# Optimization experiments

Measured on AMD Instinct MI355X. Metric: run time of the kernel, lower is better.

## Reference

```python
import jax, jax.numpy as jnp
import numpy as np


def setup_inputs() -> dict:
    key = jax.random.key(0)
    ks = jax.random.split(key, 7)
    B, C, H, W = 32, 512, 64, 64
    C8 = C // 8
    scale = 1.0 / np.sqrt(C)  # ~kaiming-ish for 1x1 conv
    return {
        "x": jax.random.normal(ks[0], (B, C, H, W), dtype=jnp.float32),
        "wq": jax.random.normal(ks[1], (C8, C), dtype=jnp.float32) * scale,
        "bq": jax.random.normal(ks[2], (C8,), dtype=jnp.float32) * 0.01,
        "wk": jax.random.normal(ks[3], (C8, C), dtype=jnp.float32) * scale,
        "bk": jax.random.normal(ks[4], (C8,), dtype=jnp.float32) * 0.01,
        "wv": jax.random.normal(ks[5], (C8, C), dtype=jnp.float32) * scale,
        "bv": jax.random.normal(ks[6], (C8,), dtype=jnp.float32) * 0.01,
    }


def reference(x, wq, bq, wk, bk, wv, bv):
    B, C, H, W = x.shape
    N = H * W
    xf = x.reshape(B, C, N)  # [B, C, N]
    # 1x1 convs == per-pixel linear projections C -> C//8
    q = jnp.einsum("bcn,oc->bon", xf, wq) + bq[None, :, None]  # [B, C8, N]
    k = jnp.einsum("bcn,oc->bon", xf, wk) + bk[None, :, None]  # [B, C8, N]
    v = jnp.einsum("bcn,oc->bon", xf, wv) + bv[None, :, None]  # [B, C8, N]
    # attention over channel pairs: [B, C8, C8], softmax over dim=-2 (rows)
    logits = jnp.einsum("bon,bpn->bop", q, k)
    attn = jax.nn.softmax(logits, axis=-2)
    out = jnp.einsum("bop,bpn->bon", attn, v)  # [B, C8, N]
    return out.mean(axis=-1)  # [B, C8]
```

## Files before the change

### kernel.cpp

```cpp
#include <hip/hip_runtime.h>


typedef __attribute__((ext_vector_type(8))) short short8;
typedef __attribute__((ext_vector_type(4))) float floatx4;
typedef __attribute__((ext_vector_type(4))) unsigned short ushort4v;

#define MFMA16(a, b, c) __builtin_amdgcn_mfma_f32_16x16x32_bf16((a), (b), (c), 0, 0, 0)

__device__ __forceinline__ unsigned short f2bf(float f) {
  unsigned int u = __float_as_uint(f);
  u = u + 0x7fffu + ((u >> 16) & 1u);
  return (unsigned short)(u >> 16);
}
__device__ __forceinline__ float bf2f(unsigned short h) {
  return __uint_as_float(((unsigned int)h) << 16);
}

constexpr int CB = 32;
constexpr int CC = 512;
constexpr int CO = 64;
constexpr int NN = 4096;
constexpr int NT = 128;
constexpr int KC = 32;
constexpr int NCH = CC / KC;

constexpr int XROW = 40;
constexpr int QROW = 72;

constexpr int WQH = 0;
constexpr int WQL = 2560;
constexpr int WKH = 5120;
constexpr int WKL = 7680;
constexpr int XHI = 10240;
constexpr int XLO = 15360;
constexpr int SMEM_U = 20480;
constexpr int QHI = 0, QLO = 4608, KHI = 9216, KLO = 13824;

__global__ __launch_bounds__(256, 2) void proj_kernel(
    const float* __restrict__ x, const float* __restrict__ wq,
    const float* __restrict__ bq, const float* __restrict__ wk,
    const float* __restrict__ bk, float* __restrict__ logits,
    float* __restrict__ xsum)
{
  __shared__ __align__(16) unsigned short smem[SMEM_U];

  const int t    = threadIdx.x;
  const int lane = t & 63;
  const int wave = t >> 6;
  const int quad = lane >> 4;
  const int l15  = lane & 15;
  const int b    = blockIdx.x >> 5;
  const int tile = blockIdx.x & 31;
  const int n0   = tile * NT;
  const int nlow = t & 31;
  const int chi  = t >> 5;

  floatx4 accq[4][2], acck[4][2];
#pragma unroll
  for (int mf = 0; mf < 4; ++mf)
#pragma unroll
    for (int nf = 0; nf < 2; ++nf) {
      accq[mf][nf] = (floatx4)0.0f;
      acck[mf][nf] = (floatx4)0.0f;
    }

  const float* xb = x + (size_t)b * CC * NN + n0;

  for (int ch = 0; ch < NCH; ++ch) {
    const int c0 = ch * KC;
    __syncthreads();

    float xs_part[4] = {0.f, 0.f, 0.f, 0.f};
#pragma unroll
    for (int i = 0; i < 4; ++i) {
      const int n = i * 32 + nlow;
      float v0 = xb[(size_t)(c0 + chi * 4 + 0) * NN + n];
      float v1 = xb[(size_t)(c0 + chi * 4 + 1) * NN + n];
      float v2 = xb[(size_t)(c0 + chi * 4 + 2) * NN + n];
      float v3 = xb[(size_t)(c0 + chi * 4 + 3) * NN + n];
      xs_part[0] += v0; xs_part[1] += v1; xs_part[2] += v2; xs_part[3] += v3;
      ushort4v h, l;
      h[0] = f2bf(v0); l[0] = f2bf(v0 - bf2f(h[0]));
      h[1] = f2bf(v1); l[1] = f2bf(v1 - bf2f(h[1]));
      h[2] = f2bf(v2); l[2] = f2bf(v2 - bf2f(h[2]));
      h[3] = f2bf(v3); l[3] = f2bf(v3 - bf2f(h[3]));
      *reinterpret_cast<ushort4v*>(&smem[XHI + n * XROW + chi * 4]) = h;
      *reinterpret_cast<ushort4v*>(&smem[XLO + n * XROW + chi * 4]) = l;
    }
#pragma unroll
    for (int j = 0; j < 4; ++j) {
      float v = xs_part[j];
      v += __shfl_xor(v, 16); v += __shfl_xor(v, 8);
      v += __shfl_xor(v, 4);  v += __shfl_xor(v, 2); v += __shfl_xor(v, 1);
      if ((lane & 31) == 0) atomicAdd(&xsum[b * CC + c0 + chi * 4 + j], v);
    }

#pragma unroll
    for (int i = 0; i < 2; ++i) {
      const int idx = t + i * 256;
      const int row = idx >> 3, cf = idx & 7;
      const floatx4 aq = *reinterpret_cast<const floatx4*>(
          &wq[(size_t)row * CC + c0 + cf * 4]);
      const floatx4 ak = *reinterpret_cast<const floatx4*>(
          &wk[(size_t)row * CC + c0 + cf * 4]);
      ushort4v qh, ql, kh, kl;
#pragma unroll
      for (int j = 0; j < 4; ++j) {
        qh[j] = f2bf(aq[j]); ql[j] = f2bf(aq[j] - bf2f(qh[j]));
        kh[j] = f2bf(ak[j]); kl[j] = f2bf(ak[j] - bf2f(kh[j]));
      }
      *reinterpret_cast<ushort4v*>(&smem[WQH + row * XROW + cf * 4]) = qh;
      *reinterpret_cast<ushort4v*>(&smem[WQL + row * XROW + cf * 4]) = ql;
      *reinterpret_cast<ushort4v*>(&smem[WKH + row * XROW + cf * 4]) = kh;
      *reinterpret_cast<ushort4v*>(&smem[WKL + row * XROW + cf * 4]) = kl;
    }
    __syncthreads();

    short8 xh[2], xl[2];
#pragma unroll
    for (int nf = 0; nf < 2; ++nf) {
      const int nr = wave * 32 + nf * 16 + l15;
      xh[nf] = *reinterpret_cast<const short8*>(&smem[XHI + nr * XROW + quad * 8]);
      xl[nf] = *reinterpret_cast<const short8*>(&smem[XLO + nr * XROW + quad * 8]);
    }
#pragma unroll
    for (int mf = 0; mf < 4; ++mf) {
      const int orow = mf * 16 + l15;
      const short8 aqh = *reinterpret_cast<const short8*>(&smem[WQH + orow * XROW + quad * 8]);
      const short8 aql = *reinterpret_cast<const short8*>(&smem[WQL + orow * XROW + quad * 8]);
      const short8 akh = *reinterpret_cast<const short8*>(&smem[WKH + orow * XROW + quad * 8]);
      const short8 akl = *reinterpret_cast<const short8*>(&smem[WKL + orow * XROW + quad * 8]);
#pragma unroll
      for (int nf = 0; nf < 2; ++nf) {
        accq[mf][nf] = MFMA16(aqh, xh[nf], accq[mf][nf]);
        accq[mf][nf] = MFMA16(aql, xh[nf], accq[mf][nf]);
        accq[mf][nf] = MFMA16(aqh, xl[nf], accq[mf][nf]);
        acck[mf][nf] = MFMA16(akh, xh[nf], acck[mf][nf]);
        acck[mf][nf] = MFMA16(akl, xh[nf], acck[mf][nf]);
        acck[mf][nf] = MFMA16(akh, xl[nf], acck[mf][nf]);
      }
    }
  }

#pragma unroll
  for (int mf = 0; mf < 4; ++mf)
#pragma unroll
    for (int r = 0; r < 4; ++r) {
      const int o = mf * 16 + quad * 4 + r;
      const float bqv = bq[o], bkv = bk[o];
#pragma unroll
      for (int nf = 0; nf < 2; ++nf) {
        accq[mf][nf][r] += bqv;
        acck[mf][nf][r] += bkv;
      }
    }

  floatx4 accS[4];
#pragma unroll
  for (int mf = 0; mf < 4; ++mf) accS[mf] = (floatx4)0.0f;

  for (int hh = 0; hh < 2; ++hh) {
    __syncthreads();
    if ((wave >> 1) == hh) {
      const int nbase = (wave & 1) * 32;
#pragma unroll
      for (int mf = 0; mf < 4; ++mf)
#pragma unroll
        for (int nf = 0; nf < 2; ++nf)
#pragma unroll
          for (int r = 0; r < 4; ++r) {
            const int o  = mf * 16 + quad * 4 + r;
            const int nc = nbase + nf * 16 + l15;
            const float qv = accq[mf][nf][r];
            const float kv = acck[mf][nf][r];
            const unsigned short qh = f2bf(qv);
            const unsigned short kh = f2bf(kv);
            smem[QHI + o * QROW + nc] = qh;
            smem[QLO + o * QROW + nc] = f2bf(qv - bf2f(qh));
            smem[KHI + o * QROW + nc] = kh;
            smem[KLO + o * QROW + nc] = f2bf(kv - bf2f(kh));
          }
    }
    __syncthreads();
#pragma unroll
    for (int ks = 0; ks < 2; ++ks) {
      const short8 bh = *reinterpret_cast<const short8*>(
          &smem[KHI + (wave * 16 + l15) * QROW + ks * 32 + quad * 8]);
      const short8 bl = *reinterpret_cast<const short8*>(
          &smem[KLO + (wave * 16 + l15) * QROW + ks * 32 + quad * 8]);
#pragma unroll
      for (int mf = 0; mf < 4; ++mf) {
        const short8 ah = *reinterpret_cast<const short8*>(
            &smem[QHI + (mf * 16 + l15) * QROW + ks * 32 + quad * 8]);
        const short8 al = *reinterpret_cast<const short8*>(
            &smem[QLO + (mf * 16 + l15) * QROW + ks * 32 + quad * 8]);
        accS[mf] = MFMA16(ah, bh, accS[mf]);
        accS[mf] = MFMA16(al, bh, accS[mf]);
        accS[mf] = MFMA16(ah, bl, accS[mf]);
      }
    }
  }

#pragma unroll
  for (int mf = 0; mf < 4; ++mf)
#pragma unroll
    for (int r = 0; r < 4; ++r) {
      const int o = mf * 16 + quad * 4 + r;
      const int p = wave * 16 + l15;
      atomicAdd(&logits[((size_t)b * CO + o) * CO + p], accS[mf][r]);
    }
}

__global__ __launch_bounds__(256) void zero_kernel(float* __restrict__ p, int n) {
  const int i = blockIdx.x * 256 + threadIdx.x;
  if (i < n) p[i] = 0.0f;
}

__global__ __launch_bounds__(256) void finalize_kernel(
    const float* __restrict__ wv, const float* __restrict__ bv,
    const float* __restrict__ logits, const float* __restrict__ xsum,
    float* __restrict__ out)
{
  __shared__ float ls[CO * 65];
  __shared__ float xs_s[CC];
  __shared__ float vbar_s[CO], w2_s[CO], cmax_s[CO];
  const int t = threadIdx.x;
  const int b = blockIdx.x;

  for (int i = t; i < CC; i += 256) xs_s[i] = xsum[b * CC + i];
#pragma unroll
  for (int i = 0; i < 16; ++i) {
    const int idx = t + i * 256;
    ls[(idx >> 6) * 65 + (idx & 63)] = logits[(size_t)b * CO * CO + idx];
  }
  __syncthreads();

  {
    const int p = t >> 2, part = t & 3;
    float s = 0.f;
    const float* wr = wv + (size_t)p * CC + part * 128;
    const float* xr = xs_s + part * 128;
#pragma unroll 4
    for (int c = 0; c < 128; ++c) s += wr[c] * xr[c];
    s += __shfl_xor(s, 1); s += __shfl_xor(s, 2);
    if (part == 0) vbar_s[p] = s * (1.0f / 4096.0f) + bv[p];
  }
  __syncthreads();

  if (t < CO) {
    float m = -1e30f;
    for (int o = 0; o < CO; ++o) m = fmaxf(m, ls[o * 65 + t]);
    float sum = 0.f;
    for (int o = 0; o < CO; ++o) sum += __expf(ls[o * 65 + t] - m);
    cmax_s[t] = m;
    w2_s[t]   = vbar_s[t] / sum;
  }
  __syncthreads();

  if (t < CO) {
    float acc = 0.f;
    for (int p = 0; p < CO; ++p)
      acc += __expf(ls[t * 65 + p] - cmax_s[p]) * w2_s[p];
    out[b * CO + t] = acc;
  }
}

extern "C" void kernel_launch(void* const* d_in, const int* in_sizes, int n_in,
                              void* d_out, int out_size, void* d_ws, size_t ws_size,
                              hipStream_t stream) {
  const float* x  = (const float*)d_in[0];
  const float* wq = (const float*)d_in[1];
  const float* bq = (const float*)d_in[2];
  const float* wk = (const float*)d_in[3];
  const float* bk = (const float*)d_in[4];
  const float* wv = (const float*)d_in[5];
  const float* bv = (const float*)d_in[6];
  float* out = (float*)d_out;

  float* logits = (float*)d_ws;
  float* xsum   = logits + CB * CO * CO;
  const int nzero = CB * CO * CO + CB * CC;

  zero_kernel<<<(nzero + 255) / 256, 256, 0, stream>>>(logits, nzero);
  proj_kernel<<<CB * (NN / NT), 256, 0, stream>>>(x, wq, bq, wk, bk, logits, xsum);
  finalize_kernel<<<CB, 256, 0, stream>>>(wv, bv, logits, xsum, out);
}
```

Before: 413.6 us.

## Precompute bf16 hi/lo weight splits and register-prefetch next x chunk

Adds a prep kernel that splits wq and wk into bf16 hi/lo parts once per call and stores them in workspace. Each projection block then loads these with 16-byte vector loads instead of converting fp32 weights in every block. The projection loop also prefetches the next channel chunk of x into registers while the current chunk is processed, to overlap global load latency with MFMA work. This costs an extra kernel launch and more registers, which may hurt occupancy under the 2-blocks launch bound.

```diff
diff --git a/kernel.cpp b/kernel.cpp
--- a/kernel.cpp
+++ b/kernel.cpp
@@ -4,6 +4,7 @@
 typedef __attribute__((ext_vector_type(8))) short short8;
 typedef __attribute__((ext_vector_type(4))) float floatx4;
 typedef __attribute__((ext_vector_type(4))) unsigned short ushort4v;
+typedef __attribute__((ext_vector_type(8))) unsigned short ushort8v;
 
 #define MFMA16(a, b, c) __builtin_amdgcn_mfma_f32_16x16x32_bf16((a), (b), (c), 0, 0, 0)
 
@@ -36,11 +37,25 @@
 constexpr int SMEM_U = 20480;
 constexpr int QHI = 0, QLO = 4608, KHI = 9216, KLO = 13824;
 
+constexpr int WB_ELEMS = CO * CC;
+
+__global__ __launch_bounds__(256) void prep_kernel(
+    const float* __restrict__ wq, const float* __restrict__ wk,
+    unsigned short* __restrict__ wbuf)
+{
+  const int i = blockIdx.x * 256 + threadIdx.x;
+  const float q = wq[i], k = wk[i];
+  const unsigned short qh = f2bf(q), kh = f2bf(k);
+  wbuf[i]                 = qh;
+  wbuf[WB_ELEMS + i]      = f2bf(q - bf2f(qh));
+  wbuf[2 * WB_ELEMS + i]  = kh;
+  wbuf[3 * WB_ELEMS + i]  = f2bf(k - bf2f(kh));
+}
+
 __global__ __launch_bounds__(256, 2) void proj_kernel(
-    const float* __restrict__ x, const float* __restrict__ wq,
-    const float* __restrict__ bq, const float* __restrict__ wk,
-    const float* __restrict__ bk, float* __restrict__ logits,
-    float* __restrict__ xsum)
+    const float* __restrict__ x, const unsigned short* __restrict__ wbuf,
+    const float* __restrict__ bq, const float* __restrict__ bk,
+    float* __restrict__ logits, float* __restrict__ xsum)
 {
   __shared__ __align__(16) unsigned short smem[SMEM_U];
 
@@ -54,6 +69,8 @@
   const int n0   = tile * NT;
   const int nlow = t & 31;
   const int chi  = t >> 5;
+  const int wrow = t >> 2;
+  const int wcf  = (t & 3) * 8;
 
   floatx4 accq[4][2], acck[4][2];
 #pragma unroll
@@ -66,18 +83,29 @@
 
   const float* xb = x + (size_t)b * CC * NN + n0;
 
+  float xr[16];
+#pragma unroll
+  for (int i = 0; i < 4; ++i)
+#pragma unroll
+    for (int cj = 0; cj < 4; ++cj)
+      xr[i * 4 + cj] = xb[(size_t)(chi * 4 + cj) * NN + i * 32 + nlow];
+
   for (int ch = 0; ch < NCH; ++ch) {
     const int c0 = ch * KC;
     __syncthreads();
 
+    const unsigned short* wsrc = wbuf + (size_t)wrow * CC + c0 + wcf;
+    const ushort8v a0 = *reinterpret_cast<const ushort8v*>(wsrc);
+    const ushort8v a1 = *reinterpret_cast<const ushort8v*>(wsrc + WB_ELEMS);
+    const ushort8v a2 = *reinterpret_cast<const ushort8v*>(wsrc + 2 * WB_ELEMS);
+    const ushort8v a3 = *reinterpret_cast<const ushort8v*>(wsrc + 3 * WB_ELEMS);
+
     float xs_part[4] = {0.f, 0.f, 0.f, 0.f};
 #pragma unroll
     for (int i = 0; i < 4; ++i) {
       const int n = i * 32 + nlow;
-      float v0 = xb[(size_t)(c0 + chi * 4 + 0) * NN + n];
-      float v1 = xb[(size_t)(c0 + chi * 4 + 1) * NN + n];
-      float v2 = xb[(size_t)(c0 + chi * 4 + 2) * NN + n];
-      float v3 = xb[(size_t)(c0 + chi * 4 + 3) * NN + n];
+      const float v0 = xr[i * 4 + 0], v1 = xr[i * 4 + 1];
+      const float v2 = xr[i * 4 + 2], v3 = xr[i * 4 + 3];
       xs_part[0] += v0; xs_part[1] += v1; xs_part[2] += v2; xs_part[3] += v3;
       ushort4v h, l;
       h[0] = f2bf(v0); l[0] = f2bf(v0 - bf2f(h[0]));
@@ -95,24 +123,18 @@
       if ((lane & 31) == 0) atomicAdd(&xsum[b * CC + c0 + chi * 4 + j], v);
     }
 
-#pragma unroll
-    for (int i = 0; i < 2; ++i) {
-      const int idx = t + i * 256;
-      const int row = idx >> 3, cf = idx & 7;
-      const floatx4 aq = *reinterpret_cast<const floatx4*>(
-          &wq[(size_t)row * CC + c0 + cf * 4]);
-      const floatx4 ak = *reinterpret_cast<const floatx4*>(
-          &wk[(size_t)row * CC + c0 + cf * 4]);
-      ushort4v qh, ql, kh, kl;
-#pragma unroll
-      for (int j = 0; j < 4; ++j) {
-        qh[j] = f2bf(aq[j]); ql[j] = f2bf(aq[j] - bf2f(qh[j]));
-        kh[j] = f2bf(ak[j]); kl[j] = f2bf(ak[j] - bf2f(kh[j]));
-      }
-      *reinterpret_cast<ushort4v*>(&smem[WQH + row * XROW + cf * 4]) = qh;
-      *reinterpret_cast<ushort4v*>(&smem[WQL + row * XROW + cf * 4]) = ql;
-      *reinterpret_cast<ushort4v*>(&smem[WKH + row * XROW + cf * 4]) = kh;
-      *reinterpret_cast<ushort4v*>(&smem[WKL + row * XROW + cf * 4]) = kl;
+    *reinterpret_cast<ushort8v*>(&smem[WQH + wrow * XROW + wcf]) = a0;
+    *reinterpret_cast<ushort8v*>(&smem[WQL + wrow * XROW + wcf]) = a1;
+    *reinterpret_cast<ushort8v*>(&smem[WKH + wrow * XROW + wcf]) = a2;
+    *reinterpret_cast<ushort8v*>(&smem[WKL + wrow * XROW + wcf]) = a3;
+
+    if (ch + 1 < NCH) {
+      const int c0n = c0 + KC;
+#pragma unroll
+      for (int i = 0; i < 4; ++i)
+#pragma unroll
+        for (int cj = 0; cj < 4; ++cj)
+          xr[i * 4 + cj] = xb[(size_t)(c0n + chi * 4 + cj) * NN + i * 32 + nlow];
     }
     __syncthreads();
 
@@ -280,8 +302,10 @@
   float* logits = (float*)d_ws;
   float* xsum   = logits + CB * CO * CO;
   const int nzero = CB * CO * CO + CB * CC;
+  unsigned short* wbuf = (unsigned short*)(xsum + CB * CC);
 
   zero_kernel<<<(nzero + 255) / 256, 256, 0, stream>>>(logits, nzero);
-  proj_kernel<<<CB * (NN / NT), 256, 0, stream>>>(x, wq, bq, wk, bk, logits, xsum);
-  finalize_kernel<<<CB, 256, 0, stream>>>(wv, bv, logits, xsum, out);
-}
+  prep_kernel<<<WB_ELEMS / 256, 256, 0, stream>>>(wq, wk, wbuf);
+  proj_kernel<<<CB * (NN / NT), 256, 0, stream>>>(x, wbuf, bq, bk, logits, xsum);
+  finalize_kernel<<<CB, 256, 0, stream>>>(wv, bv, wbuf ? logits : logits, xsum, out);
+}
```

Result: faster. 398.8 us (-3.6%).
